# Optimization experiments

Hardware: AMD Instinct MI355X
Metric: run time of the kernel (lower is better)

The kernel has to match this reference:

```python
import jax, jax.numpy as jnp
import numpy as np

N0, N1, N2 = 200000, 50000, 10000
E0, E1 = 800000, 160000
IN_DIM, H1, H2, EMB = 256, 256, 256, 128


def gcn_layer(h_src, src_idx, dst_idx, n_src, n_dst, W, b):
    # DGL GraphConv, norm='both': D_dst^{-1/2} A D_src^{-1/2} X W + b,
    # degrees clamped to min 1 (allow_zero_in_degree=True -> zero rows stay zero).
    ones = jnp.ones(src_idx.shape[0], dtype=h_src.dtype)
    out_deg = jnp.clip(jax.ops.segment_sum(ones, src_idx, num_segments=n_src), 1.0)
    in_deg = jnp.clip(jax.ops.segment_sum(ones, dst_idx, num_segments=n_dst), 1.0)
    # in_dim >= out_dim here, so DGL multiplies by W first then aggregates;
    # result is identical either way.
    h = (h_src * jax.lax.rsqrt(out_deg)[:, None]) @ W          # [n_src, out]
    agg = jax.ops.segment_sum(h[src_idx], dst_idx, num_segments=n_dst)  # [n_dst, out]
    return agg * jax.lax.rsqrt(in_deg)[:, None] + b


def setup_inputs() -> dict:
    key = jax.random.key(0)
    ks = jax.random.split(key, 10)
    h = jax.random.normal(ks[0], (N0, IN_DIM), dtype=jnp.float32)
    src0 = jax.random.randint(ks[1], (E0,), 0, N0, dtype=jnp.int32)
    dst0 = jax.random.randint(ks[2], (E0,), 0, N1, dtype=jnp.int32)
    src1 = jax.random.randint(ks[3], (E1,), 0, N1, dtype=jnp.int32)
    dst1 = jax.random.randint(ks[4], (E1,), 0, N2, dtype=jnp.int32)
    s1 = 1.0 / np.sqrt(IN_DIM)
    s2 = 1.0 / np.sqrt(H1)
    sp = 1.0 / np.sqrt(H2)
    W1 = jax.random.normal(ks[5], (IN_DIM, H1), dtype=jnp.float32) * s1
    W2 = jax.random.normal(ks[6], (H1, H2), dtype=jnp.float32) * s2
    Wp = jax.random.normal(ks[7], (H2, EMB), dtype=jnp.float32) * sp
    b1 = jnp.zeros((H1,), dtype=jnp.float32)
    b2 = jnp.zeros((H2,), dtype=jnp.float32)
    bp = jnp.zeros((EMB,), dtype=jnp.float32)
    return {"h": h, "src0": src0, "dst0": dst0, "src1": src1, "dst1": dst1,
            "W1": W1, "b1": b1, "W2": W2, "b2": b2, "Wp": Wp, "bp": bp}


def reference(h, src0, dst0, src1, dst1, W1, b1, W2, b2, Wp, bp):
    h = gcn_layer(h, src0, dst0, N0, N1, W1, b1)   # [N1, H1]
    h = gcn_layer(h, src1, dst1, N1, N2, W2, b2)   # [N2, H2]
    return h @ Wp + bp                             # [N2, EMB]
```

## Files before the change

### kernel.cpp

```cpp
#include <hip/hip_runtime.h>
#include <cstddef>

#define N0 200000
#define N1 50000
#define N2 10000
#define E0 800000
#define E1 160000

__global__ void count_kernel(const int* __restrict__ src, const int* __restrict__ dst,
                             int* __restrict__ out_cnt, int* __restrict__ in_cnt,
                             int* __restrict__ rank, int E) {
    int e = blockIdx.x * 256 + threadIdx.x;
    if (e < E) {
        atomicAdd(&out_cnt[src[e]], 1);
        rank[e] = atomicAdd(&in_cnt[dst[e]], 1);
    }
}

__global__ void scales_kernel(const int* __restrict__ cnt, float* __restrict__ rs, int n) {
    int i = blockIdx.x * 256 + threadIdx.x;
    if (i < n) rs[i] = rsqrtf((float)max(cnt[i], 1));
}

__global__ __launch_bounds__(1024) void scan_kernel(const int* __restrict__ cnt,
                                                    int* __restrict__ rowptr, int n) {
    __shared__ int partial[1024];
    const int t = threadIdx.x;
    const int chunk = (n + 1023) / 1024;
    const int begin = t * chunk;
    const int end = min(begin + chunk, n);
    int sum = 0;
    for (int i = begin; i < end; i++) sum += cnt[i];
    partial[t] = sum;
    __syncthreads();
    for (int off = 1; off < 1024; off <<= 1) {
        int v = (t >= off) ? partial[t - off] : 0;
        __syncthreads();
        partial[t] += v;
        __syncthreads();
    }
    int run = partial[t] - sum;
    for (int i = begin; i < end; i++) {
        rowptr[i] = run;
        run += cnt[i];
    }
    if (t == 1023) rowptr[n] = partial[1023];
}

__global__ void fill_kernel(const int* __restrict__ src, const int* __restrict__ dst,
                            const int* __restrict__ rank, const int* __restrict__ rowptr,
                            int* __restrict__ csr, int E) {
    int e = blockIdx.x * 256 + threadIdx.x;
    if (e < E) csr[rowptr[dst[e]] + rank[e]] = src[e];
}

__global__ __launch_bounds__(256) void gather_kernel(const float* __restrict__ hsrc,
                                                     const float* __restrict__ rs_src,
                                                     const int* __restrict__ rowptr,
                                                     const int* __restrict__ csr,
                                                     float* __restrict__ agg, int n_dst) {
    int w    = (blockIdx.x * 256 + threadIdx.x) >> 6;
    int lane = threadIdx.x & 63;
    if (w >= n_dst) return;
    int e   = rowptr[w];
    int end = rowptr[w + 1];
    float4 acc = make_float4(0.f, 0.f, 0.f, 0.f);
    for (; e + 1 < end; e += 2) {
        int s0 = csr[e];
        int s1 = csr[e + 1];
        float sc0 = rs_src[s0];
        float sc1 = rs_src[s1];
        float4 v0 = ((const float4*)(hsrc + (size_t)s0 * 256))[lane];
        float4 v1 = ((const float4*)(hsrc + (size_t)s1 * 256))[lane];
        acc.x += v0.x * sc0; acc.y += v0.y * sc0; acc.z += v0.z * sc0; acc.w += v0.w * sc0;
        acc.x += v1.x * sc1; acc.y += v1.y * sc1; acc.z += v1.z * sc1; acc.w += v1.w * sc1;
    }
    if (e < end) {
        int s0 = csr[e];
        float sc0 = rs_src[s0];
        float4 v0 = ((const float4*)(hsrc + (size_t)s0 * 256))[lane];
        acc.x += v0.x * sc0; acc.y += v0.y * sc0; acc.z += v0.z * sc0; acc.w += v0.w * sc0;
    }
    ((float4*)(agg + (size_t)w * 256))[lane] = acc;
}

__global__ __launch_bounds__(256) void gemm_k256(const float* __restrict__ A,
                                                 const float* __restrict__ rs,
                                                 const float* __restrict__ B,
                                                 const float* __restrict__ bias,
                                                 float* __restrict__ C, int M, int N) {
    __shared__ float As[16][64];
    __shared__ float Bs[16][64];

    const int tidx = threadIdx.x;
    const int tx = tidx & 15;
    const int ty = tidx >> 4;
    const int rowBase = blockIdx.x * 64;
    const int colBase = blockIdx.y * 64;

    const int arow = tidx >> 2;
    const int kch  = tidx & 3;
    const int grow = min(rowBase + arow, M - 1);
    const float scale = rs ? rs[grow] : 1.0f;
    const float* Arow = A + (size_t)grow * 256;

    const int bk = tidx >> 4;
    const int bc = tidx & 15;

    float acc[4][4];
#pragma unroll
    for (int i = 0; i < 4; i++)
#pragma unroll
        for (int j = 0; j < 4; j++) acc[i][j] = 0.0f;

    for (int kb = 0; kb < 256; kb += 16) {
        float4 a = *(const float4*)(Arow + kb + kch * 4);
        a.x *= scale; a.y *= scale; a.z *= scale; a.w *= scale;
        As[kch * 4 + 0][arow] = a.x;
        As[kch * 4 + 1][arow] = a.y;
        As[kch * 4 + 2][arow] = a.z;
        As[kch * 4 + 3][arow] = a.w;
        float4 b = *(const float4*)(B + (size_t)(kb + bk) * N + colBase + bc * 4);
        *(float4*)&Bs[bk][bc * 4] = b;
        __syncthreads();

#pragma unroll
        for (int kk = 0; kk < 16; kk++) {
            float4 af = ((const float4*)As[kk])[ty];
            float4 bf = ((const float4*)Bs[kk])[tx];
            acc[0][0] += af.x * bf.x; acc[0][1] += af.x * bf.y; acc[0][2] += af.x * bf.z; acc[0][3] += af.x * bf.w;
            acc[1][0] += af.y * bf.x; acc[1][1] += af.y * bf.y; acc[1][2] += af.y * bf.z; acc[1][3] += af.y * bf.w;
            acc[2][0] += af.z * bf.x; acc[2][1] += af.z * bf.y; acc[2][2] += af.z * bf.z; acc[2][3] += af.z * bf.w;
            acc[3][0] += af.w * bf.x; acc[3][1] += af.w * bf.y; acc[3][2] += af.w * bf.z; acc[3][3] += af.w * bf.w;
        }
        __syncthreads();
    }

    float4 bias4 = ((const float4*)(bias + colBase))[tx];
#pragma unroll
    for (int i = 0; i < 4; i++) {
        int row = rowBase + ty * 4 + i;
        if (row < M) {
            float4 o;
            o.x = acc[i][0] + bias4.x;
            o.y = acc[i][1] + bias4.y;
            o.z = acc[i][2] + bias4.z;
            o.w = acc[i][3] + bias4.w;
            *(float4*)(C + (size_t)row * N + colBase + tx * 4) = o;
        }
    }
}

extern "C" void kernel_launch(void* const* d_in, const int* in_sizes, int n_in,
                              void* d_out, int out_size, void* d_ws, size_t ws_size,
                              hipStream_t stream) {
    const float* h    = (const float*)d_in[0];
    const int*   src0 = (const int*)d_in[1];
    const int*   dst0 = (const int*)d_in[2];
    const int*   src1 = (const int*)d_in[3];
    const int*   dst1 = (const int*)d_in[4];
    const float* W1   = (const float*)d_in[5];
    const float* b1   = (const float*)d_in[6];
    const float* W2   = (const float*)d_in[7];
    const float* b2   = (const float*)d_in[8];
    const float* Wp   = (const float*)d_in[9];
    const float* bp   = (const float*)d_in[10];
    float* out = (float*)d_out;

    int* ib = (int*)d_ws;
    int* cnt_out0 = ib;
    int* cnt_in0  = cnt_out0 + N0;
    int* cnt_out1 = cnt_in0 + N1;
    int* cnt_in1  = cnt_out1 + N1;
    int* rank0    = cnt_in1 + N2;
    int* rank1    = rank0 + E0;
    int* rowptr0  = rank1 + E1;
    int* rowptr1  = rowptr0 + (N1 + 1);
    int* csr0     = rowptr1 + (N2 + 1);
    int* csr1     = csr0 + E0;
    int* iend     = csr1 + E1;
    float* fb = (float*)(ib + 2290004);
    float* rs_out0 = fb;
    float* rs_in0  = rs_out0 + N0;
    float* rs_out1 = rs_in0 + N1;
    float* rs_in1  = rs_out1 + N1;
    float* h1      = rs_in1 + N2 + 0;
    float* regA    = h1 + (size_t)N1 * 256;
    float* agg0    = regA;
    float* agg1    = regA;
    float* h2      = regA + 3200000;
    (void)iend;

    const int n_cnt = N0 + N1 + N1 + N2;

    hipMemsetAsync(cnt_out0, 0, (size_t)n_cnt * sizeof(int), stream);

    count_kernel<<<(E0 + 255) / 256, 256, 0, stream>>>(src0, dst0, cnt_out0, cnt_in0, rank0, E0);
    count_kernel<<<(E1 + 255) / 256, 256, 0, stream>>>(src1, dst1, cnt_out1, cnt_in1, rank1, E1);

    scales_kernel<<<(n_cnt + 255) / 256, 256, 0, stream>>>(cnt_out0, rs_out0, n_cnt);

    scan_kernel<<<1, 1024, 0, stream>>>(cnt_in0, rowptr0, N1);
    scan_kernel<<<1, 1024, 0, stream>>>(cnt_in1, rowptr1, N2);

    fill_kernel<<<(E0 + 255) / 256, 256, 0, stream>>>(src0, dst0, rank0, rowptr0, csr0, E0);
    fill_kernel<<<(E1 + 255) / 256, 256, 0, stream>>>(src1, dst1, rank1, rowptr1, csr1, E1);

    gather_kernel<<<(N1 + 3) / 4, 256, 0, stream>>>(h, rs_out0, rowptr0, csr0, agg0, N1);

    gemm_k256<<<dim3((N1 + 63) / 64, 4), 256, 0, stream>>>(agg0, rs_in0, W1, b1, h1, N1, 256);

    gather_kernel<<<(N2 + 3) / 4, 256, 0, stream>>>(h1, rs_out1, rowptr1, csr1, agg1, N2);

    gemm_k256<<<dim3((N2 + 63) / 64, 4), 256, 0, stream>>>(agg1, rs_in1, W2, b2, h2, N2, 256);

    gemm_k256<<<dim3((N2 + 63) / 64, 2), 256, 0, stream>>>(h2, nullptr, Wp, bp, out, N2, 128);
}
```

Before: 749.0 us.

## Replace FP32 tiled GEMMs with bf16 MFMA GEMMs and fuse dst scaling into gather

The shared-memory FP32 GEMMs are replaced by a register-only kernel that converts A rows to bf16 on the fly and uses 16x16x32 bf16 MFMA instructions. The weights are pre-packed into the MFMA fragment layout by a small kernel. The destination-degree scale moves into the gather, and the gather loop is unrolled by four for more memory parallelism. Reducing inputs to bf16 lowers precision and may change results beyond tolerance, and the GEMM reads A directly from global memory without LDS reuse.

Result: faster. 711.6 us (-5.0%).

```diff
diff --git a/kernel.cpp b/kernel.cpp
--- a/kernel.cpp
+++ b/kernel.cpp
@@ -6,6 +6,15 @@
 #define N2 10000
 #define E0 800000
 #define E1 160000
+
+typedef short bf16x8 __attribute__((ext_vector_type(8)));
+typedef float f32x4 __attribute__((ext_vector_type(4)));
+
+__device__ __forceinline__ unsigned short f2bf(float f) {
+    unsigned int u = __float_as_uint(f);
+    unsigned int r = (u + 0x7FFF + ((u >> 16) & 1)) >> 16;
+    return (unsigned short)r;
+}
 
 __global__ void count_kernel(const int* __restrict__ src, const int* __restrict__ dst,
                              int* __restrict__ out_cnt, int* __restrict__ in_cnt,
@@ -56,6 +65,7 @@
 
 __global__ __launch_bounds__(256) void gather_kernel(const float* __restrict__ hsrc,
                                                      const float* __restrict__ rs_src,
+                                                     const float* __restrict__ rs_dst,
                                                      const int* __restrict__ rowptr,
                                                      const int* __restrict__ csr,
                                                      float* __restrict__ agg, int n_dst) {
@@ -65,88 +75,102 @@
     int e   = rowptr[w];
     int end = rowptr[w + 1];
     float4 acc = make_float4(0.f, 0.f, 0.f, 0.f);
-    for (; e + 1 < end; e += 2) {
-        int s0 = csr[e];
-        int s1 = csr[e + 1];
-        float sc0 = rs_src[s0];
-        float sc1 = rs_src[s1];
+    for (; e + 3 < end; e += 4) {
+        int s0 = csr[e], s1 = csr[e + 1], s2 = csr[e + 2], s3 = csr[e + 3];
+        float sc0 = rs_src[s0], sc1 = rs_src[s1], sc2 = rs_src[s2], sc3 = rs_src[s3];
         float4 v0 = ((const float4*)(hsrc + (size_t)s0 * 256))[lane];
         float4 v1 = ((const float4*)(hsrc + (size_t)s1 * 256))[lane];
+        float4 v2 = ((const float4*)(hsrc + (size_t)s2 * 256))[lane];
+        float4 v3 = ((const float4*)(hsrc + (size_t)s3 * 256))[lane];
         acc.x += v0.x * sc0; acc.y += v0.y * sc0; acc.z += v0.z * sc0; acc.w += v0.w * sc0;
         acc.x += v1.x * sc1; acc.y += v1.y * sc1; acc.z += v1.z * sc1; acc.w += v1.w * sc1;
-    }
-    if (e < end) {
+        acc.x += v2.x * sc2; acc.y += v2.y * sc2; acc.z += v2.z * sc2; acc.w += v2.w * sc2;
+        acc.x += v3.x * sc3; acc.y += v3.y * sc3; acc.z += v3.z * sc3; acc.w += v3.w * sc3;
+    }
+    for (; e < end; e++) {
         int s0 = csr[e];
         float sc0 = rs_src[s0];
         float4 v0 = ((const float4*)(hsrc + (size_t)s0 * 256))[lane];
         acc.x += v0.x * sc0; acc.y += v0.y * sc0; acc.z += v0.z * sc0; acc.w += v0.w * sc0;
     }
+    float sd = rs_dst[w];
+    acc.x *= sd; acc.y *= sd; acc.z *= sd; acc.w *= sd;
     ((float4*)(agg + (size_t)w * 256))[lane] = acc;
 }
 
-__global__ __launch_bounds__(256) void gemm_k256(const float* __restrict__ A,
-                                                 const float* __restrict__ rs,
-                                                 const float* __restrict__ B,
+__global__ void pack_b_kernel(const float* __restrict__ W, unsigned short* __restrict__ Bp,
+                              int K, int N) {
+    int tid = blockIdx.x * 256 + threadIdx.x;
+    int total = (N / 16) * (K / 32) * 64;
+    if (tid >= total) return;
+    int lane = tid & 63;
+    int rest = tid >> 6;
+    int s  = rest % (K / 32);
+    int ct = rest / (K / 32);
+    int col = ct * 16 + (lane & 15);
+    int k0  = s * 32 + (lane >> 4) * 8;
+    unsigned short* dst = Bp + (size_t)tid * 8;
+#pragma unroll
+    for (int j = 0; j < 8; j++) dst[j] = f2bf(W[(size_t)(k0 + j) * N + col]);
+}
+
+template <int NCT>
+__global__ __launch_bounds__(256) void gemm_mfma(const float* __restrict__ A,
+                                                 const unsigned short* __restrict__ Bp,
                                                  const float* __restrict__ bias,
                                                  float* __restrict__ C, int M, int N) {
-    __shared__ float As[16][64];
-    __shared__ float Bs[16][64];
-
-    const int tidx = threadIdx.x;
-    const int tx = tidx & 15;
-    const int ty = tidx >> 4;
+    const int lane = threadIdx.x & 63;
+    const int wave = threadIdx.x >> 6;
     const int rowBase = blockIdx.x * 64;
-    const int colBase = blockIdx.y * 64;
-
-    const int arow = tidx >> 2;
-    const int kch  = tidx & 3;
-    const int grow = min(rowBase + arow, M - 1);
-    const float scale = rs ? rs[grow] : 1.0f;
-    const float* Arow = A + (size_t)grow * 256;
-
-    const int bk = tidx >> 4;
-    const int bc = tidx & 15;
-
-    float acc[4][4];
-#pragma unroll
-    for (int i = 0; i < 4; i++)
-#pragma unroll
-        for (int j = 0; j < 4; j++) acc[i][j] = 0.0f;
-
-    for (int kb = 0; kb < 256; kb += 16) {
-        float4 a = *(const float4*)(Arow + kb + kch * 4);
-        a.x *= scale; a.y *= scale; a.z *= scale; a.w *= scale;
-        As[kch * 4 + 0][arow] = a.x;
-        As[kch * 4 + 1][arow] = a.y;
-        As[kch * 4 + 2][arow] = a.z;
-        As[kch * 4 + 3][arow] = a.w;
-        float4 b = *(const float4*)(B + (size_t)(kb + bk) * N + colBase + bc * 4);
-        *(float4*)&Bs[bk][bc * 4] = b;
-        __syncthreads();
-
-#pragma unroll
-        for (int kk = 0; kk < 16; kk++) {
-            float4 af = ((const float4*)As[kk])[ty];
-            float4 bf = ((const float4*)Bs[kk])[tx];
-            acc[0][0] += af.x * bf.x; acc[0][1] += af.x * bf.y; acc[0][2] += af.x * bf.z; acc[0][3] += af.x * bf.w;
-            acc[1][0] += af.y * bf.x; acc[1][1] += af.y * bf.y; acc[1][2] += af.y * bf.z; acc[1][3] += af.y * bf.w;
-            acc[2][0] += af.z * bf.x; acc[2][1] += af.z * bf.y; acc[2][2] += af.z * bf.z; acc[2][3] += af.z * bf.w;
-            acc[3][0] += af.w * bf.x; acc[3][1] += af.w * bf.y; acc[3][2] += af.w * bf.z; acc[3][3] += af.w * bf.w;
+    const int colBase = wave * (NCT * 16);
+    const int lm = lane & 15;
+    const int quad = lane >> 4;
+
+    f32x4 acc[4][NCT];
+#pragma unroll
+    for (int rt = 0; rt < 4; rt++)
+#pragma unroll
+        for (int ct = 0; ct < NCT; ct++) acc[rt][ct] = (f32x4){0.f, 0.f, 0.f, 0.f};
+
+    const float* ap[4];
+#pragma unroll
+    for (int rt = 0; rt < 4; rt++) {
+        int r = min(rowBase + rt * 16 + lm, M - 1);
+        ap[rt] = A + (size_t)r * 256 + quad * 8;
+    }
+
+#pragma unroll
+    for (int s = 0; s < 8; s++) {
+        bf16x8 afrag[4];
+#pragma unroll
+        for (int rt = 0; rt < 4; rt++) {
+            const float* p = ap[rt] + s * 32;
+            float4 x = *(const float4*)p;
+            float4 y = *(const float4*)(p + 4);
+            union { unsigned short u[8]; bf16x8 v; } af;
+            af.u[0] = f2bf(x.x); af.u[1] = f2bf(x.y); af.u[2] = f2bf(x.z); af.u[3] = f2bf(x.w);
+            af.u[4] = f2bf(y.x); af.u[5] = f2bf(y.y); af.u[6] = f2bf(y.z); af.u[7] = f2bf(y.w);
+            afrag[rt] = af.v;
         }
-        __syncthreads();
-    }
-
-    float4 bias4 = ((const float4*)(bias + colBase))[tx];
-#pragma unroll
-    for (int i = 0; i < 4; i++) {
-        int row = rowBase + ty * 4 + i;
-        if (row < M) {
-            float4 o;
-            o.x = acc[i][0] + bias4.x;
-            o.y = acc[i][1] + bias4.y;
-            o.z = acc[i][2] + bias4.z;
-            o.w = acc[i][3] + bias4.w;
-            *(float4*)(C + (size_t)row * N + colBase + tx * 4) = o;
+#pragma unroll
+        for (int ct = 0; ct < NCT; ct++) {
+            bf16x8 bfrag = *(const bf16x8*)(Bp + (((size_t)(wave * NCT + ct) * 8 + s) * 64 + lane) * 8);
+#pragma unroll
+            for (int rt = 0; rt < 4; rt++)
+                acc[rt][ct] = __builtin_amdgcn_mfma_f32_16x16x32_bf16(afrag[rt], bfrag, acc[rt][ct], 0, 0, 0);
+        }
+    }
+
+#pragma unroll
+    for (int ct = 0; ct < NCT; ct++) {
+        float bv = bias[colBase + ct * 16 + lm];
+#pragma unroll
+        for (int rt = 0; rt < 4; rt++) {
+#pragma unroll
+            for (int i = 0; i < 4; i++) {
+                int row = rowBase + rt * 16 + quad * 4 + i;
+                if (row < M) C[(size_t)row * N + colBase + ct * 16 + lm] = acc[rt][ct][i] + bv;
+            }
         }
     }
 }
@@ -178,22 +202,27 @@
     int* rowptr1  = rowptr0 + (N1 + 1);
     int* csr0     = rowptr1 + (N2 + 1);
     int* csr1     = csr0 + E0;
-    int* iend     = csr1 + E1;
     float* fb = (float*)(ib + 2290004);
     float* rs_out0 = fb;
     float* rs_in0  = rs_out0 + N0;
     float* rs_out1 = rs_in0 + N1;
     float* rs_in1  = rs_out1 + N1;
-    float* h1      = rs_in1 + N2 + 0;
+    float* h1      = rs_in1 + N2;
     float* regA    = h1 + (size_t)N1 * 256;
     float* agg0    = regA;
     float* agg1    = regA;
     float* h2      = regA + 3200000;
-    (void)iend;
+    unsigned short* W1p = (unsigned short*)(regA + (size_t)N1 * 256);
+    unsigned short* W2p = W1p + 256 * 256;
+    unsigned short* Wpp = W2p + 256 * 256;
 
     const int n_cnt = N0 + N1 + N1 + N2;
 
     hipMemsetAsync(cnt_out0, 0, (size_t)n_cnt * sizeof(int), stream);
+
+    pack_b_kernel<<<(16 * 8 * 64 + 255) / 256, 256, 0, stream>>>(W1, W1p, 256, 256);
+    pack_b_kernel<<<(16 * 8 * 64 + 255) / 256, 256, 0, stream>>>(W2, W2p, 256, 256);
+    pack_b_kernel<<<(8 * 8 * 64 + 255) / 256, 256, 0, stream>>>(Wp, Wpp, 256, 128);
 
     count_kernel<<<(E0 + 255) / 256, 256, 0, stream>>>(src0, dst0, cnt_out0, cnt_in0, rank0, E0);
     count_kernel<<<(E1 + 255) / 256, 256, 0, stream>>>(src1, dst1, cnt_out1, cnt_in1, rank1, E1);
@@ -206,13 +235,13 @@
     fill_kernel<<<(E0 + 255) / 256, 256, 0, stream>>>(src0, dst0, rank0, rowptr0, csr0, E0);
     fill_kernel<<<(E1 + 255) / 256, 256, 0, stream>>>(src1, dst1, rank1, rowptr1, csr1, E1);
 
-    gather_kernel<<<(N1 + 3) / 4, 256, 0, stream>>>(h, rs_out0, rowptr0, csr0, agg0, N1);
-
-    gemm_k256<<<dim3((N1 + 63) / 64, 4), 256, 0, stream>>>(agg0, rs_in0, W1, b1, h1, N1, 256);
-
-    gather_kernel<<<(N2 + 3) / 4, 256, 0, stream>>>(h1, rs_out1, rowptr1, csr1, agg1, N2);
-
-    gemm_k256<<<dim3((N2 + 63) / 64, 4), 256, 0, stream>>>(agg1, rs_in1, W2, b2, h2, N2, 256);
-
-    gemm_k256<<<dim3((N2 + 63) / 64, 2), 256, 0, stream>>>(h2, nullptr, Wp, bp, out, N2, 128);
-}
+    gather_kernel<<<(N1 + 3) / 4, 256, 0, stream>>>(h, rs_out0, rs_in0, rowptr0, csr0, agg0, N1);
+
+    gemm_mfma<4><<<(N1 + 63) / 64, 256, 0, stream>>>(agg0, W1p, b1, h1, N1, 256);
+
+    gather_kernel<<<(N2 + 3) / 4, 256, 0, stream>>>(h1, rs_out1, rs_in1, rowptr1, csr1, agg1, N2);
+
+    gemm_mfma<4><<<(N2 + 63) / 64, 256, 0, stream>>>(agg1, W2p, b2, h2, N2, 256);
+
+    gemm_mfma<2><<<(N2 + 63) / 64, 256, 0, stream>>>(h2, Wpp, bp, out, N2, 128);
+}
```
